# Kernel tuning notes

Hardware: AMD Instinct MI355X
Metric: run time of the kernel (lower is better)

## Reference

```python
import jax, jax.numpy as jnp
import numpy as np

B, N, XD = 64, 512, 32  # batch, n_points, x_dims (feature columns); last 2 cols are t, y


def setup_inputs() -> dict:
    key = jax.random.key(0)
    xtys = jax.random.normal(key, (B, N, XD + 2), dtype=jnp.float32)
    return {"xtys": xtys}


def _linear_dml(xtys):
    b, n, D = xtys.shape
    d = D - 2
    xs = xtys[..., :d]          # (b, n, d) covariates
    ts = xtys[..., d]           # (b, n)   treatment
    ys = xtys[..., d + 1]       # (b, n)   outcome

    # Growing-prefix least squares via cumulative sufficient statistics.
    # For prefix i (rows 0..i): min-norm lstsq solution w = pinv(X^T X) X^T v == pinv(X) v,
    # matching torch.linalg.lstsq (gelsy/gelsd) semantics including rank-deficient prefixes.
    G = jnp.cumsum(jnp.einsum('bnd,bne->bnde', xs, xs), axis=1)      # (b,n,d,d) Gram
    Xty = jnp.cumsum(xs * ys[..., None], axis=1)                     # (b,n,d)
    Xtt = jnp.cumsum(xs * ts[..., None], axis=1)                     # (b,n,d)
    Sty = jnp.cumsum(ts * ys, axis=1)                                # (b,n)
    Stt = jnp.cumsum(ts * ts, axis=1)                                # (b,n)

    Ginv = jnp.linalg.pinv(G)                                        # batched pinv, (b,n,d,d)
    wy = jnp.einsum('bnde,bne->bnd', Ginv, Xty)
    wt = jnp.einsum('bnde,bne->bnd', Ginv, Xtt)

    # ate_i = <t_res, y_res> / <t_res, t_res> over prefix, expanded via the stats above.
    num = (Sty
           - jnp.einsum('bnd,bnd->bn', wt, Xty)
           - jnp.einsum('bnd,bnd->bn', wy, Xtt)
           + jnp.einsum('bnd,bnde,bne->bn', wt, G, wy))
    den = (Stt
           - 2.0 * jnp.einsum('bnd,bnd->bn', wt, Xtt)
           + jnp.einsum('bnd,bnde,bne->bn', wt, G, wt))
    safe = den > 0
    ate = jnp.where(safe, num / jnp.where(safe, den, 1.0), 0.0)      # min-norm: 0 when thats==0

    means = ate.at[:, 0].set(0.0)                                    # i==0 special case
    stds = jnp.zeros_like(means)                                     # module always appends zeros
    return means, 2.0 * jnp.log(stds)                                # -> -inf, as in the original


def reference(xtys):
    return _linear_dml(xtys)
```

## Files before the change

kernel.cpp:

```cpp
#include <hip/hip_runtime.h>
#include <math.h>
#include <utility>

#define BB 64
#define NN 512
#define DD 32
#define ZD 34
#define NE 595
#define WIN 8
#define NW 64
#define WACT 60

#define SEG 4
#define RS 128
#define KWS 16
#define CH 4
#define ECH 149
#define PSTRIDE 17

__device__ inline void ent2ij(int e, int& i, int& j) {
    int ii = 0, rem = e;
    while (rem >= ZD - ii) { rem -= (ZD - ii); ++ii; }
    i = ii; j = ii + rem;
}

template<int N> struct Pack { Pack<N - 1> head; float v; };
template<> struct Pack<1> { float v; };
template<int I, int N> __device__ __forceinline__ float& pget(Pack<N>& p) {
    static_assert(I < N, "oob");
    if constexpr (I == N - 1) return p.v;
    else return pget<I, N - 1>(p.head);
}

__device__ __forceinline__ float rdlane(float x, int srclane) {
    return __int_as_float(__builtin_amdgcn_readlane(__float_as_int(x), srclane));
}

__global__ __launch_bounds__(256) void dml_gram(const float* __restrict__ xtys,
                                                float* __restrict__ P,
                                                float* __restrict__ out) {
    const int t   = threadIdx.x;
    const int blk = blockIdx.x;
    const int c   = blk % CH;
    const int bg  = blk / CH;
    const int g   = bg % SEG;
    const int b   = bg / SEG;

    const int gid = blk * 256 + t;
    if (gid < BB * NN) out[BB * NN + gid] = 0.0f;
    if (gid < BB * DD) out[(gid >> 5) * NN + (gid & 31)] = 0.0f;

    __shared__ float zs[RS * ZD];
    const float* src = xtys + ((size_t)b * NN + (size_t)g * RS) * ZD;
    for (int u = t; u < RS * ZD; u += 256) zs[u] = src[u];
    __syncthreads();

    const int e = c * ECH + t;
    if (t < ECH && e < NE) {
        int i, j;
        ent2ij(e, i, j);
        float* pdst = P + (size_t)(b * SEG + g) * PSTRIDE * NE + e;
        double acc = 0.0;
#pragma unroll
        for (int k = 0; k < KWS; ++k) {
            pdst[k * NE] = (float)acc;
#pragma unroll
            for (int s8 = 0; s8 < WIN; ++s8) {
                const float* row = &zs[(k * WIN + s8) * ZD];
                acc = fma((double)row[i], (double)row[j], acc);
            }
        }
        pdst[KWS * NE] = (float)acc;
    }
}


template<int R> __device__ __forceinline__
float initval(int j, const float* snL, const float* zb) {
    if constexpr (R < DD) {
        float v = 0.0f;
        if (j < DD) {
            int i0 = (R < j) ? R : j;
            int j0 = (R < j) ? j : R;
            v = snL[i0 * ZD - (i0 * (i0 - 1)) / 2 + (j0 - i0)];
        } else if (j < DD + WIN) {
            v = zb[(j - DD) * ZD + R];
        } else if (j == 40) {
            v = snL[R * ZD - (R * (R - 1)) / 2 + (DD - R)];
        } else if (j == 41) {
            v = snL[R * ZD - (R * (R - 1)) / 2 + (DD + 1 - R)];
        }
        return v;
    } else if constexpr (R < DD + WIN) {
        return (j < DD) ? zb[(R - DD) * ZD + j] : 0.0f;
    } else if constexpr (R == 40) {
        return (j < DD) ? snL[j * ZD - (j * (j - 1)) / 2 + (DD - j)] : 0.0f;
    } else if constexpr (R == 41) {
        return (j < DD) ? snL[j * ZD - (j * (j - 1)) / 2 + (DD + 1 - j)] : 0.0f;
    } else {
        return 0.0f;
    }
}
template<int R> __device__ __forceinline__
void init_rec(Pack<48>& A, int j, const float* snL, const float* zb) {
    if constexpr (R < 48) {
        pget<R>(A) = initval<R>(j, snL, zb);
        init_rec<R + 1>(A, j, snL, zb);
    }
}

template<int K, int R> __device__ __forceinline__
void elim_rows(Pack<48>& A, float t) {
    if constexpr (R < DD + 10) {
        float fr = rdlane(pget<R>(A), K);
        pget<R>(A) = fmaf(-fr, t, pget<R>(A));
        elim_rows<K, R + 1>(A, t);
    }
}
template<int K> __device__ __forceinline__
void elim_step(Pack<48>& A) {
    float piv  = rdlane(pget<K>(A), K);
    float invp = (piv > 1e-30f) ? 1.0f / piv : 0.0f;
    float t    = invp * pget<K>(A);
    elim_rows<K, K + 1>(A, t);
}
template<int... Ks> __device__ __forceinline__
void elim_all(Pack<48>& A, std::integer_sequence<int, Ks...>) {
    ((elim_step<Ks>(A)), ...);
}

template<int R> __device__ __forceinline__
void kdump(Pack<48>& A, float* Kl, int c) {
    if constexpr (R < DD + 10) {
        Kl[(R - DD) * 10 + c] = -pget<R>(A);
        kdump<R + 1>(A, Kl, c);
    }
}

template<int L> __device__ __forceinline__
void tinit(Pack<96>& T, int m, const float* Kl, const float* zb) {
    if constexpr (L < 96) {
        constexpr int I = L / 12, J = L % 12;
        float v;
        if constexpr (J < 8) {
            float kij = (I < m && J < m) ? Kl[I * 10 + J] : 0.0f;
            v = kij + ((I == J) ? 1.0f : 0.0f);
        } else if constexpr (J == 8)  v = (I < m) ? Kl[I * 10 + 8] : 0.0f;
        else if constexpr (J == 9)    v = (I < m) ? zb[I * ZD + DD] : 0.0f;
        else if constexpr (J == 10)   v = (I < m) ? Kl[I * 10 + 9] : 0.0f;
        else                          v = (I < m) ? zb[I * ZD + DD + 1] : 0.0f;
        pget<L>(T) = v;
        tinit<L + 1>(T, m, Kl, zb);
    }
}
template<int K, int I, int J> __device__ __forceinline__
void gj_cols(Pack<96>& T, float f) {
    if constexpr (J < 12) {
        pget<I * 12 + J>(T) = fmaf(-f, pget<K * 12 + J>(T), pget<I * 12 + J>(T));
        gj_cols<K, I, J + 1>(T, f);
    }
}
template<int K, int I> __device__ __forceinline__
void gj_rows(Pack<96>& T, float invp) {
    if constexpr (I < 8) {
        if constexpr (I != K) {
            float f = pget<I * 12 + K>(T) * invp;
            gj_cols<K, I, K + 1>(T, f);
        }
        gj_rows<K, I + 1>(T, invp);
    }
}
template<int K> __device__ __forceinline__
void gj_step(Pack<96>& T) {
    float piv  = pget<K * 12 + K>(T);
    float invp = (piv > 1e-30f || piv < -1e-30f) ? 1.0f / piv : 0.0f;
    gj_rows<K, 0>(T, invp);
}
template<int... Ks> __device__ __forceinline__
void gj_all(Pack<96>& T, std::integer_sequence<int, Ks...>) {
    ((gj_step<Ks>(T)), ...);
}
template<int I> __device__ __forceinline__
void finacc(Pack<96>& T, int m, const float* Kl, const float* zb,
            double& dt, double& nt) {
    if constexpr (I < 8) {
        if (I < m) {
            float di   = pget<I * 12 + I>(T);
            float dinv = (di > 1e-30f || di < -1e-30f) ? 1.0f / di : 0.0f;
            double s1 = (double)(pget<I * 12 + 8>(T) * dinv);
            double s2 = (double)(pget<I * 12 + 9>(T) * dinv);
            double r1 = (double)(pget<I * 12 + 10>(T) * dinv);
            double r2 = (double)(pget<I * 12 + 11>(T) * dinv);
            double g  = (double)Kl[80 + I] - (double)zb[I * ZD + DD];
            dt += g * (s1 - s2);
            nt += g * (r1 - r2);
        }
        finacc<I + 1>(T, m, Kl, zb, dt, nt);
    }
}

__global__ __launch_bounds__(64) void dml_solve(const float* __restrict__ xtys,
                                                const float* __restrict__ P,
                                                float* __restrict__ out) {
    const int id   = blockIdx.x;
    const int w    = (id % WACT) + 4;
    const int b    = id / WACT;
    const int lane = threadIdx.x;
    const int g    = w >> 4;
    const int k    = w & 15;

    __shared__ float snL[NE];
    __shared__ float zb[WIN * ZD];
    __shared__ float Kl[100];

    const float* pb  = P + (size_t)b * SEG * PSTRIDE * NE;
    const float* src = xtys + ((size_t)b * NN + (size_t)w * WIN) * ZD;
    for (int u = lane; u < NE; u += 64) {
        float v = pb[(size_t)(g * PSTRIDE + k) * NE + u];
        for (int g2 = 0; g2 < g; ++g2)
            v += pb[(size_t)(g2 * PSTRIDE + KWS) * NE + u];
        snL[u] = v;
    }
    for (int u = lane; u < WIN * ZD; u += 64) zb[u] = src[u];
    __syncthreads();

    Pack<48> A;
    init_rec<0>(A, lane, snL, zb);

    elim_all(A, std::make_integer_sequence<int, DD>{});

    if (lane >= DD && lane < DD + 10) kdump<DD>(A, Kl, lane - DD);
    __syncthreads();

    if (lane < 8) {
        const int m = lane + 1;
        Pack<96> T;
        tinit<0>(T, m, Kl, zb);
        gj_all(T, std::make_integer_sequence<int, 8>{});
        double dt = 0.0, nt = 0.0;
        finacc<0>(T, m, Kl, zb, dt, nt);
        double Stt0 = (double)snL[592];
        double Sty0 = (double)snL[593];
        double den  = Stt0 - (double)Kl[88] + dt;
        double num  = Sty0 - (double)Kl[89] + nt;
        double val  = (den > 0.0) ? num / den : 0.0;
        if (!isfinite(val)) val = 0.0;
        out[b * NN + w * WIN + lane] = (float)val;
    }
}

extern "C" void kernel_launch(void* const* d_in, const int* in_sizes, int n_in,
                              void* d_out, int out_size, void* d_ws, size_t ws_size,
                              hipStream_t stream) {
    const float* xtys = (const float*)d_in[0];
    float* out = (float*)d_out;
    float* P = (float*)d_ws;

    hipLaunchKernelGGL(dml_gram, dim3(BB * SEG * CH), dim3(256), 0, stream, xtys, P, out);
    hipLaunchKernelGGL(dml_solve, dim3(BB * WACT), dim3(64), 0, stream, xtys, P, out);
}
```

Before: 103.7 us.

## Register-tile Gram prefix sums as 2x2 blocks and resegment rows into 8 chunks

```diff
diff --git a/kernel.cpp b/kernel.cpp
--- a/kernel.cpp
+++ b/kernel.cpp
@@ -11,17 +11,20 @@
 #define NW 64
 #define WACT 60
 
-#define SEG 4
-#define RS 128
-#define KWS 16
-#define CH 4
-#define ECH 149
-#define PSTRIDE 17
-
-__device__ inline void ent2ij(int e, int& i, int& j) {
-    int ii = 0, rem = e;
-    while (rem >= ZD - ii) { rem -= (ZD - ii); ++ii; }
+#define SEG 8
+#define RS 64
+#define KWS 8
+#define NT 153
+#define PSTRIDE 9
+
+__device__ inline void tile2ij(int t, int& i, int& j) {
+    int ii = 0, rem = t;
+    while (rem >= 17 - ii) { rem -= (17 - ii); ++ii; }
     i = ii; j = ii + rem;
+}
+
+__device__ __forceinline__ int eidx(int i, int j) {
+    return i * ZD - (i * (i - 1)) / 2 + (j - i);
 }
 
 template<int N> struct Pack { Pack<N - 1> head; float v; };
@@ -41,36 +44,52 @@
                                                 float* __restrict__ out) {
     const int t   = threadIdx.x;
     const int blk = blockIdx.x;
-    const int c   = blk % CH;
-    const int bg  = blk / CH;
-    const int g   = bg % SEG;
-    const int b   = bg / SEG;
+    const int g   = blk % SEG;
+    const int b   = blk / SEG;
 
     const int gid = blk * 256 + t;
     if (gid < BB * NN) out[BB * NN + gid] = 0.0f;
     if (gid < BB * DD) out[(gid >> 5) * NN + (gid & 31)] = 0.0f;
 
-    __shared__ float zs[RS * ZD];
-    const float* src = xtys + ((size_t)b * NN + (size_t)g * RS) * ZD;
-    for (int u = t; u < RS * ZD; u += 256) zs[u] = src[u];
+    __shared__ float2 zs2[RS * 17];
+    const float2* src2 = (const float2*)(xtys + ((size_t)b * NN + (size_t)g * RS) * ZD);
+    for (int u = t; u < RS * 17; u += 256) zs2[u] = src2[u];
     __syncthreads();
 
-    const int e = c * ECH + t;
-    if (t < ECH && e < NE) {
-        int i, j;
-        ent2ij(e, i, j);
-        float* pdst = P + (size_t)(b * SEG + g) * PSTRIDE * NE + e;
-        double acc = 0.0;
+    if (t < NT) {
+        int ti, tj;
+        tile2ij(t, ti, tj);
+        const int i    = 2 * ti, j = 2 * tj;
+        const bool dia = (ti == tj);
+        const int eA   = eidx(i, j);
+        const int eB   = dia ? eidx(i + 1, i + 1)
+                             : eidx(i + 1, j);
+
+        float* pdst = P + (size_t)blk * PSTRIDE * NE;
+        double a00 = 0.0, a01 = 0.0, a10 = 0.0, a11 = 0.0;
 #pragma unroll
         for (int k = 0; k < KWS; ++k) {
-            pdst[k * NE] = (float)acc;
+            float* ps = pdst + k * NE;
+            ps[eA]     = (float)a00;
+            ps[eA + 1] = (float)a01;
+            if (dia) { ps[eB] = (float)a11; }
+            else     { ps[eB] = (float)a10; ps[eB + 1] = (float)a11; }
 #pragma unroll
             for (int s8 = 0; s8 < WIN; ++s8) {
-                const float* row = &zs[(k * WIN + s8) * ZD];
-                acc = fma((double)row[i], (double)row[j], acc);
+                const int s = k * WIN + s8;
+                float2 xa = zs2[s * 17 + ti];
+                float2 xb = zs2[s * 17 + tj];
+                a00 = fma((double)xa.x, (double)xb.x, a00);
+                a01 = fma((double)xa.x, (double)xb.y, a01);
+                a10 = fma((double)xa.y, (double)xb.x, a10);
+                a11 = fma((double)xa.y, (double)xb.y, a11);
             }
         }
-        pdst[KWS * NE] = (float)acc;
+        float* ps = pdst + KWS * NE;
+        ps[eA]     = (float)a00;
+        ps[eA + 1] = (float)a01;
+        if (dia) { ps[eB] = (float)a11; }
+        else     { ps[eB] = (float)a10; ps[eB + 1] = (float)a11; }
     }
 }
 
@@ -206,8 +225,8 @@
     const int w    = (id % WACT) + 4;
     const int b    = id / WACT;
     const int lane = threadIdx.x;
-    const int g    = w >> 4;
-    const int k    = w & 15;
+    const int g    = w >> 3;
+    const int k    = w & 7;
 
     __shared__ float snL[NE];
     __shared__ float zb[WIN * ZD];
@@ -256,6 +275,6 @@
     float* out = (float*)d_out;
     float* P = (float*)d_ws;
 
-    hipLaunchKernelGGL(dml_gram, dim3(BB * SEG * CH), dim3(256), 0, stream, xtys, P, out);
+    hipLaunchKernelGGL(dml_gram, dim3(BB * SEG), dim3(256), 0, stream, xtys, P, out);
     hipLaunchKernelGGL(dml_solve, dim3(BB * WACT), dim3(64), 0, stream, xtys, P, out);
 }
```

Measured after the change: 107.7 us. 3.8% more time.
